# Performance work log

Measured on AMD Instinct MI355X. Metric: run time of the kernel, lower is better.

Reference implementation:

```python
import jax, jax.numpy as jnp
import numpy as np

C = 64          # residual channels
N_LAYERS = 30
MAX_STEPS = 200
SQRT2 = 2.0 ** 0.5


def _conv1d(x, W, b, dilation=1, pad=0):
    # x: [B, Cin, T], W: [Cout, Cin, K], b: [Cout]
    y = jax.lax.conv_general_dilated(
        x, W, window_strides=(1,), padding=[(pad, pad)],
        rhs_dilation=(dilation,), dimension_numbers=('NCH', 'OIH', 'NCH'))
    return y + b[None, :, None]


def _silu(x):
    return x * jax.nn.sigmoid(x)


def _emb_table():
    steps = jnp.arange(MAX_STEPS, dtype=jnp.float32)[:, None]      # [200,1]
    dims = jnp.arange(64, dtype=jnp.float32)[None, :]              # [1,64]
    t = steps * 10.0 ** (dims * 4.0 / 63.0)                        # [200,64]
    return jnp.concatenate([jnp.sin(t), jnp.cos(t)], axis=1)       # [200,128]


def setup_inputs() -> dict:
    key = jax.random.key(0)
    ks = jax.random.split(key, 20)
    B, T = 4, 16384
    f32 = jnp.float32
    inp = {
        'audio': jax.random.normal(ks[0], (B, 1, T), dtype=f32),
        'diffusion_step': jax.random.randint(ks[1], (B,), 0, MAX_STEPS),
        # input projection Conv1d(1, 64, 1)
        'in_W': jax.random.normal(ks[2], (C, 1, 1), f32) * 1.0,
        'in_b': jax.random.normal(ks[3], (C,), f32) * 0.01,
        # diffusion embedding MLP 128->512->512
        'p1_W': jax.random.normal(ks[4], (512, 128), f32) * (1.0 / np.sqrt(128)),
        'p1_b': jnp.zeros((512,), f32),
        'p2_W': jax.random.normal(ks[5], (512, 512), f32) * (1.0 / np.sqrt(512)),
        'p2_b': jnp.zeros((512,), f32),
        # per-layer params (stacked over 30 layers)
        'dw_W': jax.random.normal(ks[6], (N_LAYERS, 2 * C, C, 3), f32) * (1.0 / np.sqrt(3 * C)),
        'dw_b': jnp.zeros((N_LAYERS, 2 * C), f32),
        'dp_W': jax.random.normal(ks[7], (N_LAYERS, C, 512), f32) * (1.0 / np.sqrt(512)),
        'dp_b': jnp.zeros((N_LAYERS, C), f32),
        'op_W': jax.random.normal(ks[8], (N_LAYERS, 2 * C, C, 1), f32) * (1.0 / np.sqrt(C)),
        'op_b': jnp.zeros((N_LAYERS, 2 * C), f32),
        # skip projection Conv1d(64,64,1)
        'sk_W': jax.random.normal(ks[9], (C, C, 1), f32) * (1.0 / np.sqrt(C)),
        'sk_b': jnp.zeros((C,), f32),
        # output projection Conv1d(64,1,1), weight zero-init like original
        'out_W': jnp.zeros((1, C, 1), f32),
        'out_b': jax.random.normal(ks[10], (1,), f32) * 0.01,
    }
    return inp


def reference(audio, diffusion_step, in_W, in_b, p1_W, p1_b, p2_W, p2_b,
              dw_W, dw_b, dp_W, dp_b, op_W, op_b, sk_W, sk_b, out_W, out_b):
    x = jax.nn.relu(_conv1d(audio, in_W, in_b))                    # [B,64,T]
    # diffusion embedding
    t = _emb_table()[diffusion_step]                               # [B,128]
    t = _silu(t @ p1_W.T + p1_b)                                   # [B,512]
    t = _silu(t @ p2_W.T + p2_b)                                   # [B,512]
    skip = None
    for i in range(N_LAYERS):
        d = 2 ** (i % 10)
        cond = (t @ dp_W[i].T + dp_b[i])[:, :, None]               # [B,64,1]
        y = _conv1d(x + cond, dw_W[i], dw_b[i], dilation=d, pad=d) # [B,128,T]
        gate, filt = y[:, :C], y[:, C:]
        y = jax.nn.sigmoid(gate) * jnp.tanh(filt)                  # [B,64,T]
        y = _conv1d(y, op_W[i], op_b[i])                           # [B,128,T]
        residual, sk = y[:, :C], y[:, C:]
        x = (x + residual) / SQRT2
        skip = sk if skip is None else skip + sk
    x = skip / np.sqrt(float(N_LAYERS)).astype(np.float32)
    x = jax.nn.relu(_conv1d(x, sk_W, sk_b))
    return _conv1d(x, out_W, out_b)                                # [B,1,T]
```

## Files before the change

kernel.cpp:

```cpp
#include <hip/hip_runtime.h>
#include <math.h>

#define C 64
#define NL 30
#define T 16384
#define B 4

typedef __bf16 bf16_t;
typedef __bf16 bf16x8 __attribute__((ext_vector_type(8)));
typedef __bf16 bf16x4 __attribute__((ext_vector_type(4)));
typedef float f32x4 __attribute__((ext_vector_type(4)));

typedef const __attribute__((address_space(1))) unsigned int glb_u32;
typedef __attribute__((address_space(3))) unsigned int lds_u32;

constexpr float INV_SQRT2   = 0.70710678118654752440f;
constexpr float INV_SQRT_NL = 0.18257418583505537115f;

__device__ __forceinline__ float fsig(float x) {
    return __builtin_amdgcn_rcpf(1.f + __builtin_amdgcn_exp2f(-1.44269504089f * x));
}
__device__ __forceinline__ float ftanh(float x) {
    return fmaf(2.f, __builtin_amdgcn_rcpf(1.f + __builtin_amdgcn_exp2f(-2.88539008178f * x)), -1.f);
}
__device__ __forceinline__ int swz(int off) { return off ^ ((off >> 3) & 0x70); }

__global__ void pack_weights(const float* __restrict__ dw_W,
                             const float* __restrict__ op_W,
                             const float* __restrict__ sk_W,
                             bf16_t* __restrict__ convpk,
                             bf16_t* __restrict__ oppk,
                             bf16_t* __restrict__ skpk) {
    int idx = blockIdx.x * 256 + threadIdx.x;
    const int ndw = NL * 128 * 192;
    const int nop = NL * 128 * 64;
    if (idx < ndw) {
        int k = idx % 192; int r = idx / 192;
        int oc = r % 128;  int l = r / 128;
        int tap = k >> 6, ic = k & 63;
        convpk[idx] = (bf16_t)dw_W[((l * 128 + oc) * 64 + ic) * 3 + tap];
    } else if (idx < ndw + nop) {
        oppk[idx - ndw] = (bf16_t)op_W[idx - ndw];
    } else if (idx < ndw + nop + 4096) {
        int j = idx - ndw - nop;
        skpk[j] = (bf16_t)(sk_W[j] * INV_SQRT_NL);
    }
}

__global__ void cond_embp1(const int* __restrict__ step,
                           const float* __restrict__ p1_W, const float* __restrict__ p1_b,
                           float* __restrict__ h1out) {
    __shared__ float e[128];
    __shared__ float red[256];
    int b = blockIdx.x, blk = blockIdx.y, tid = threadIdx.x;
    int s = step[b];
    if (tid < 128) {
        int d = tid & 63;
        float tf = (float)s * powf(10.f, (float)d * 4.f / 63.f);
        double td = (double)tf;
        e[tid] = (tid < 64) ? (float)sin(td) : (float)cos(td);
    }
    __syncthreads();
    int ol = tid >> 2, q = tid & 3;
    int o = blk * 64 + ol;
    const float4* wr = (const float4*)(p1_W + o * 128 + q * 32);
    const float4* ev = (const float4*)(e + q * 32);
    float a = 0.f;
    #pragma unroll
    for (int j = 0; j < 8; ++j) {
        float4 wv = wr[j]; float4 xv = ev[j];
        a = fmaf(wv.x, xv.x, a); a = fmaf(wv.y, xv.y, a);
        a = fmaf(wv.z, xv.z, a); a = fmaf(wv.w, xv.w, a);
    }
    red[tid] = a;
    __syncthreads();
    if (q == 0) {
        float v = red[tid] + red[tid + 1] + red[tid + 2] + red[tid + 3] + p1_b[o];
        h1out[b * 512 + o] = v / (1.f + expf(-v));
    }
}

__global__ void cond_p2(const float* __restrict__ h1,
                        const float* __restrict__ p2_W, const float* __restrict__ p2_b,
                        float* __restrict__ h2out) {
    __shared__ float red[256];
    int b = blockIdx.x, blk = blockIdx.y, tid = threadIdx.x;
    int ol = tid >> 2, q = tid & 3;
    int o = blk * 64 + ol;
    const float4* wr = (const float4*)(p2_W + o * 512 + q * 128);
    const float4* hv = (const float4*)(h1 + b * 512 + q * 128);
    float a = 0.f;
    #pragma unroll 8
    for (int j = 0; j < 32; ++j) {
        float4 wv = wr[j]; float4 xv = hv[j];
        a = fmaf(wv.x, xv.x, a); a = fmaf(wv.y, xv.y, a);
        a = fmaf(wv.z, xv.z, a); a = fmaf(wv.w, xv.w, a);
    }
    red[tid] = a;
    __syncthreads();
    if (q == 0) {
        float v = red[tid] + red[tid + 1] + red[tid + 2] + red[tid + 3] + p2_b[o];
        h2out[b * 512 + o] = v / (1.f + expf(-v));
    }
}

__global__ void cond_stage2b(const float* __restrict__ h2,
                             const float* __restrict__ dp_W, const float* __restrict__ dp_b,
                             const bf16_t* __restrict__ convpk,
                             const float* __restrict__ dw_b,
                             float* __restrict__ bias2) {
    __shared__ float red[256];
    __shared__ float cond_s[64];
    int l = blockIdx.x, b = blockIdx.y;
    int tid = threadIdx.x;
    {
        int o = tid >> 2, q = tid & 3;
        const float4* wr = (const float4*)(dp_W + ((size_t)l * C + o) * 512 + q * 128);
        const float4* h = (const float4*)(h2 + b * 512 + q * 128);
        float a = 0.f;
        #pragma unroll 8
        for (int j = 0; j < 32; ++j) {
            float4 wv = wr[j]; float4 hv = h[j];
            a = fmaf(wv.x, hv.x, a); a = fmaf(wv.y, hv.y, a);
            a = fmaf(wv.z, hv.z, a); a = fmaf(wv.w, hv.w, a);
        }
        red[tid] = a;
        __syncthreads();
        if (q == 0)
            cond_s[o] = red[tid] + red[tid + 1] + red[tid + 2] + red[tid + 3] + dp_b[l * C + o];
    }
    __syncthreads();
    int oc = tid & 127, kh = tid >> 7;
    const bf16_t* wr = convpk + ((size_t)l * 128 + oc) * 192 + kh * 96;
    float a = kh ? 0.f : dw_b[l * 128 + oc];
    #pragma unroll
    for (int j = 0; j < 96; ++j)
        a = fmaf((float)wr[j], cond_s[(kh * 96 + j) & 63], a);
    __syncthreads();
    red[tid] = a;
    __syncthreads();
    if (tid < 128)
        bias2[(l * B + b) * 128 + tid] = red[tid] + red[tid + 128];
}

__global__ void in_conv(const float* __restrict__ audio,
                        const float* __restrict__ in_W, const float* __restrict__ in_b,
                        bf16_t* __restrict__ x) {
    int idx = blockIdx.x * 256 + threadIdx.x;
    int cb = idx & 7;
    int t = (idx >> 3) & (T - 1);
    int b = idx >> 17;
    float av = audio[b * T + t];
    bf16x8 o;
    #pragma unroll
    for (int j = 0; j < 8; ++j) {
        int c = cb * 8 + j;
        o[j] = (bf16_t)fmaxf(fmaf(in_W[c], av, in_b[c]), 0.f);
    }
    *(bf16x8*)(x + ((size_t)b * T + t) * 64 + cb * 8) = o;
}

__global__ __launch_bounds__(256) void layer_kernel(
    const bf16_t* __restrict__ x_in, bf16_t* __restrict__ x_out, bf16_t* __restrict__ skip,
    const bf16_t* __restrict__ convpk, const bf16_t* __restrict__ oppk,
    const float* __restrict__ bias2, const float* __restrict__ op_b,
    const bf16_t* __restrict__ zpage,
    int layer, int dil, int first)
{
    extern __shared__ char sm[];

    int tid = threadIdx.x;
    int w = __builtin_amdgcn_readfirstlane(tid >> 6);
    int l = tid & 63;
    int lr = l & 15;
    int g = l >> 4;
    int b = blockIdx.y;
    int tbase = blockIdx.x * 128;
    const bf16_t* xb = x_in + (size_t)b * T * 64;
    const bool dual = (dil <= 32);
    const int R = (dil <= 16) ? 3 : 4;

#define STAGE_SLAB(Sbase, t0s, RR)                                           \
    _Pragma("unroll")                                                        \
    for (int r = 0; r < (RR); ++r) {                                         \
        int row = r * 32 + (tid >> 3), c16 = tid & 7;                        \
        int ts = (t0s) - dil + row;                                          \
        int c16s = c16 ^ (row & 7);                                          \
        const bf16_t* src = ((unsigned)ts < (unsigned)T)                     \
            ? xb + (size_t)ts * 64 + c16s * 8 : zpage + c16s * 8;            \
        __builtin_amdgcn_global_load_lds((glb_u32*)src,                      \
            (lds_u32*)(sm + (Sbase) + r * 4096 + w * 1024), 16, 0, 0);       \
    }
#define STAGE_M3(t0s)                                                        \
    _Pragma("unroll")                                                        \
    for (int it = 0; it < 6; ++it) {                                         \
        int qq = it * 256 + tid;                                             \
        int slice = qq >> 9, row = (qq >> 3) & 63, c16 = qq & 7;             \
        int ts = (t0s) + row + (slice - 1) * dil;                            \
        int c16s = c16 ^ (row & 7);                                          \
        const bf16_t* src = ((unsigned)ts < (unsigned)T)                     \
            ? xb + (size_t)ts * 64 + c16s * 8 : zpage + c16s * 8;            \
        __builtin_amdgcn_global_load_lds((glb_u32*)src,                      \
            (lds_u32*)(sm + it * 4096 + w * 1024), 16, 0, 0);                \
    }

    if (dual) {
        if (dil <= 16) {
            STAGE_SLAB(0, tbase, 3)
            STAGE_SLAB(12288, tbase + 64, 3)
            asm volatile("s_waitcnt vmcnt(3)" ::: "memory");
        } else {
            STAGE_SLAB(0, tbase, 4)
            STAGE_SLAB(16384, tbase + 64, 4)
            asm volatile("s_waitcnt vmcnt(4)" ::: "memory");
        }
        __builtin_amdgcn_s_barrier();
        __builtin_amdgcn_sched_barrier(0);
    }

    bf16x8 cA[2][6];
    const bf16_t* cw = convpk + (size_t)layer * 128 * 192;
    #pragma unroll
    for (int mf = 0; mf < 2; ++mf)
        #pragma unroll
        for (int kf = 0; kf < 6; ++kf)
            cA[mf][kf] = *(const bf16x8*)(cw + (mf * 64 + w * 16 + lr) * 192 + kf * 32 + g * 8);
    bf16x8 oA[2][2];
    const bf16_t* ow = oppk + (size_t)layer * 128 * 64;
    #pragma unroll
    for (int mf = 0; mf < 2; ++mf)
        #pragma unroll
        for (int kf = 0; kf < 2; ++kf)
            oA[mf][kf] = *(const bf16x8*)(ow + (mf * 64 + w * 16 + lr) * 64 + kf * 32 + g * 8);
    f32x4 bC[2], bO[2];
    const float* b2 = bias2 + (layer * B + b) * 128;
    const float* ob = op_b + layer * 2 * C;
    #pragma unroll
    for (int mf = 0; mf < 2; ++mf)
        #pragma unroll
        for (int r = 0; r < 4; ++r) {
            bC[mf][r] = b2[mf * 64 + w * 16 + g * 4 + r];
            bO[mf][r] = ob[mf * 64 + w * 16 + g * 4 + r];
        }

    size_t bb = (size_t)b * T * 64;
    const int zb = dual ? 2 * R * 4096 : 24576;
    const int tapstride = dual ? dil * 128 : 8192;

    for (int st = 0; st < 2; ++st) {
        int Sb = dual ? st * R * 4096 : 0;
        int t0 = tbase + st * 64;

        if (!dual) {
            STAGE_M3(t0)
            __syncthreads();
        }

        f32x4 acc[2][4];
        #pragma unroll
        for (int mf = 0; mf < 2; ++mf)
            #pragma unroll
            for (int nf = 0; nf < 4; ++nf) acc[mf][nf] = bC[mf];
        #pragma unroll
        for (int kf = 0; kf < 6; ++kf) {
            int tap = kf >> 1;
            int kc = (kf & 1) * 32;
            bf16x8 Bf[4];
            #pragma unroll
            for (int nf = 0; nf < 4; ++nf) {
                int off = Sb + tap * tapstride + (nf * 16 + lr) * 128 + (kc + g * 8) * 2;
                Bf[nf] = *(const bf16x8*)(sm + swz(off));
            }
            #pragma unroll
            for (int mf = 0; mf < 2; ++mf)
                #pragma unroll
                for (int nf = 0; nf < 4; ++nf)
                    acc[mf][nf] = __builtin_amdgcn_mfma_f32_16x16x32_bf16(
                        cA[mf][kf], Bf[nf], acc[mf][nf], 0, 0, 0);
        }

        #pragma unroll
        for (int nf = 0; nf < 4; ++nf) {
            union { bf16_t hh[4]; uint2 u; } zp;
            #pragma unroll
            for (int r = 0; r < 4; ++r)
                zp.hh[r] = (bf16_t)(fsig(acc[0][nf][r]) * ftanh(acc[1][nf][r]));
            int off = zb + (nf * 16 + lr) * 128 + (w * 16 + g * 4) * 2;
            *(uint2*)(sm + swz(off)) = zp.u;
        }
        __syncthreads();

        f32x4 acc2[2][4];
        #pragma unroll
        for (int mf = 0; mf < 2; ++mf)
            #pragma unroll
            for (int nf = 0; nf < 4; ++nf) acc2[mf][nf] = bO[mf];
        #pragma unroll
        for (int kf = 0; kf < 2; ++kf) {
            bf16x8 Zf[4];
            #pragma unroll
            for (int nf = 0; nf < 4; ++nf) {
                int off = zb + (nf * 16 + lr) * 128 + (kf * 32 + g * 8) * 2;
                Zf[nf] = *(const bf16x8*)(sm + swz(off));
            }
            #pragma unroll
            for (int mf = 0; mf < 2; ++mf)
                #pragma unroll
                for (int nf = 0; nf < 4; ++nf)
                    acc2[mf][nf] = __builtin_amdgcn_mfma_f32_16x16x32_bf16(
                        oA[mf][kf], Zf[nf], acc2[mf][nf], 0, 0, 0);
        }

        #pragma unroll
        for (int nf = 0; nf < 4; ++nf) {
            int t = t0 + nf * 16 + lr;
            int c0 = w * 16 + g * 4;
            int xoff = Sb + tapstride + (nf * 16 + lr) * 128 + c0 * 2;
            bf16x4 xv = *(const bf16x4*)(sm + swz(xoff));
            bf16x4 ro, so;
            bf16_t* sp = skip + bb + (size_t)t * 64 + c0;
            if (first) {
                #pragma unroll
                for (int r = 0; r < 4; ++r) {
                    ro[r] = (bf16_t)(((float)xv[r] + acc2[0][nf][r]) * INV_SQRT2);
                    so[r] = (bf16_t)acc2[1][nf][r];
                }
            } else {
                bf16x4 sv = *(const bf16x4*)sp;
                #pragma unroll
                for (int r = 0; r < 4; ++r) {
                    ro[r] = (bf16_t)(((float)xv[r] + acc2[0][nf][r]) * INV_SQRT2);
                    so[r] = (bf16_t)((float)sv[r] + acc2[1][nf][r]);
                }
            }
            *(bf16x4*)(x_out + bb + (size_t)t * 64 + c0) = ro;
            *(bf16x4*)sp = so;
        }
        if (st == 0) __syncthreads();
    }
#undef STAGE_SLAB
#undef STAGE_M3
}

__global__ __launch_bounds__(256) void final_kernel(
    const bf16_t* __restrict__ skip, const bf16_t* __restrict__ skpk,
    const float* __restrict__ sk_b,
    const float* __restrict__ out_W, const float* __restrict__ out_b,
    float* __restrict__ out)
{
    __shared__ uint4 tile_u[512];
    __shared__ float part[16][66];
    unsigned char* sm = (unsigned char*)tile_u;
    int tid = threadIdx.x;
    int w = __builtin_amdgcn_readfirstlane(tid >> 6);
    int l = tid & 63, lr = l & 15, g = l >> 4;
    int b = blockIdx.y, t0 = blockIdx.x * 64;
    const bf16_t* sb = skip + (size_t)b * T * 64;

    #pragma unroll
    for (int it = 0; it < 2; ++it) {
        int q = it * 256 + tid;
        int row = q >> 3, c16 = q & 7;
        uint4 val = *(const uint4*)(sb + (size_t)(t0 + row) * 64 + c16 * 8);
        *(uint4*)(sm + swz(row * 128 + c16 * 16)) = val;
    }

    bf16x8 aS[2];
    #pragma unroll
    for (int kf = 0; kf < 2; ++kf)
        aS[kf] = *(const bf16x8*)(skpk + (w * 16 + lr) * 64 + kf * 32 + g * 8);
    f32x4 acc[4];
    #pragma unroll
    for (int nf = 0; nf < 4; ++nf)
        #pragma unroll
        for (int r = 0; r < 4; ++r) acc[nf][r] = sk_b[w * 16 + g * 4 + r];
    __syncthreads();

    #pragma unroll
    for (int kf = 0; kf < 2; ++kf) {
        bf16x8 Bf[4];
        #pragma unroll
        for (int nf = 0; nf < 4; ++nf) {
            int off = (nf * 16 + lr) * 128 + (kf * 32 + g * 8) * 2;
            Bf[nf] = *(const bf16x8*)(sm + swz(off));
        }
        #pragma unroll
        for (int nf = 0; nf < 4; ++nf)
            acc[nf] = __builtin_amdgcn_mfma_f32_16x16x32_bf16(aS[kf], Bf[nf], acc[nf], 0, 0, 0);
    }

    #pragma unroll
    for (int nf = 0; nf < 4; ++nf) {
        float o = 0.f;
        #pragma unroll
        for (int r = 0; r < 4; ++r)
            o = fmaf(out_W[w * 16 + g * 4 + r], fmaxf(acc[nf][r], 0.f), o);
        part[w * 4 + g][nf * 16 + lr] = o;
    }
    __syncthreads();
    if (tid < 64) {
        float o = out_b[0];
        #pragma unroll
        for (int j = 0; j < 16; ++j) o += part[j][tid];
        out[(size_t)b * T + t0 + tid] = o;
    }
}

extern "C" void kernel_launch(void* const* d_in, const int* in_sizes, int n_in,
                              void* d_out, int out_size, void* d_ws, size_t ws_size,
                              hipStream_t stream) {
    const float* audio = (const float*)d_in[0];
    const int*   dstep = (const int*)d_in[1];
    const float* in_W  = (const float*)d_in[2];
    const float* in_b  = (const float*)d_in[3];
    const float* p1_W  = (const float*)d_in[4];
    const float* p1_b  = (const float*)d_in[5];
    const float* p2_W  = (const float*)d_in[6];
    const float* p2_b  = (const float*)d_in[7];
    const float* dw_W  = (const float*)d_in[8];
    const float* dw_b  = (const float*)d_in[9];
    const float* dp_W  = (const float*)d_in[10];
    const float* dp_b  = (const float*)d_in[11];
    const float* op_W  = (const float*)d_in[12];
    const float* op_b  = (const float*)d_in[13];
    const float* sk_W  = (const float*)d_in[14];
    const float* sk_b  = (const float*)d_in[15];
    const float* out_W = (const float*)d_in[16];
    const float* out_b = (const float*)d_in[17];

    float* ws = (float*)d_ws;
    const size_t NXE = (size_t)B * T * 64;
    float* h1    = ws;
    float* h2    = h1 + B * 512;
    float* bias2 = h2 + B * 512;
    float* zpg   = bias2 + NL * B * 128;
    bf16_t* xA   = (bf16_t*)(zpg + 128);
    bf16_t* xB   = xA + NXE;
    bf16_t* skip = xB + NXE;
    bf16_t* convpk = skip + NXE;
    bf16_t* oppk   = convpk + (size_t)NL * 128 * 192;
    bf16_t* skpk   = oppk + (size_t)NL * 128 * 64;

    hipMemsetAsync(zpg, 0, 512, stream);
    hipLaunchKernelGGL(pack_weights, dim3(3856), dim3(256), 0, stream,
                       dw_W, op_W, sk_W, convpk, oppk, skpk);
    hipLaunchKernelGGL(cond_embp1, dim3(B, 8), dim3(256), 0, stream,
                       dstep, p1_W, p1_b, h1);
    hipLaunchKernelGGL(cond_p2, dim3(B, 8), dim3(256), 0, stream,
                       h1, p2_W, p2_b, h2);
    hipLaunchKernelGGL(cond_stage2b, dim3(NL, B), dim3(256), 0, stream,
                       h2, dp_W, dp_b, convpk, dw_b, bias2);
    hipLaunchKernelGGL(in_conv, dim3(B * T * 8 / 256), dim3(256), 0, stream,
                       audio, in_W, in_b, xA);
    for (int i = 0; i < NL; ++i) {
        bf16_t* xin  = (i & 1) ? xB : xA;
        bf16_t* xout = (i & 1) ? xA : xB;
        int dil = 1 << (i % 10);
        int shmem = (dil <= 16) ? 32768 : (dil <= 32 ? 40960 : 32768);
        hipLaunchKernelGGL(layer_kernel, dim3(T / 128, B), dim3(256), shmem, stream,
                           xin, xout, skip, convpk, oppk, bias2, op_b,
                           (const bf16_t*)zpg, i, dil, (i == 0) ? 1 : 0);
    }
    hipLaunchKernelGGL(final_kernel, dim3(T / 64, B), dim3(256), 0, stream,
                       skip, skpk, sk_b, out_W, out_b, (float*)d_out);
}
```

Measured before the change: 499.5 us.

## Fuse pairs of small-dilation WaveNet layers into one kernel with halo recompute

Layers with dilation up to 32 are now processed in pairs inside one templated kernel. The first layer's output, including halo rows, stays in LDS and the second layer consumes it directly, while skip contributions are accumulated in registers. This is meant to halve global round-trips of the activation and skip tensors and the number of launches for those layers, at the cost of redundant halo computation and more LDS. The remaining large-dilation layers keep a simplified three-slice staging path, and block indices are remapped to spread tiles across the grid.

```diff
diff --git a/kernel.cpp b/kernel.cpp
--- a/kernel.cpp
+++ b/kernel.cpp
@@ -167,7 +167,8 @@
     const bf16_t* __restrict__ zpage,
     int layer, int dil, int first)
 {
-    extern __shared__ char sm[];
+    __shared__ uint4 smem_u[2048];
+    char* sm = (char*)smem_u;
 
     int tid = threadIdx.x;
     int w = __builtin_amdgcn_readfirstlane(tid >> 6);
@@ -175,48 +176,10 @@
     int lr = l & 15;
     int g = l >> 4;
     int b = blockIdx.y;
-    int tbase = blockIdx.x * 128;
+    int bid = blockIdx.x;
+    int tile = ((bid & 7) << 4) + (bid >> 3);
+    int tbase = tile * 128;
     const bf16_t* xb = x_in + (size_t)b * T * 64;
-    const bool dual = (dil <= 32);
-    const int R = (dil <= 16) ? 3 : 4;
-
-#define STAGE_SLAB(Sbase, t0s, RR)                                           \
-    _Pragma("unroll")                                                        \
-    for (int r = 0; r < (RR); ++r) {                                         \
-        int row = r * 32 + (tid >> 3), c16 = tid & 7;                        \
-        int ts = (t0s) - dil + row;                                          \
-        int c16s = c16 ^ (row & 7);                                          \
-        const bf16_t* src = ((unsigned)ts < (unsigned)T)                     \
-            ? xb + (size_t)ts * 64 + c16s * 8 : zpage + c16s * 8;            \
-        __builtin_amdgcn_global_load_lds((glb_u32*)src,                      \
-            (lds_u32*)(sm + (Sbase) + r * 4096 + w * 1024), 16, 0, 0);       \
-    }
-#define STAGE_M3(t0s)                                                        \
-    _Pragma("unroll")                                                        \
-    for (int it = 0; it < 6; ++it) {                                         \
-        int qq = it * 256 + tid;                                             \
-        int slice = qq >> 9, row = (qq >> 3) & 63, c16 = qq & 7;             \
-        int ts = (t0s) + row + (slice - 1) * dil;                            \
-        int c16s = c16 ^ (row & 7);                                          \
-        const bf16_t* src = ((unsigned)ts < (unsigned)T)                     \
-            ? xb + (size_t)ts * 64 + c16s * 8 : zpage + c16s * 8;            \
-        __builtin_amdgcn_global_load_lds((glb_u32*)src,                      \
-            (lds_u32*)(sm + it * 4096 + w * 1024), 16, 0, 0);                \
-    }
-
-    if (dual) {
-        if (dil <= 16) {
-            STAGE_SLAB(0, tbase, 3)
-            STAGE_SLAB(12288, tbase + 64, 3)
-            asm volatile("s_waitcnt vmcnt(3)" ::: "memory");
-        } else {
-            STAGE_SLAB(0, tbase, 4)
-            STAGE_SLAB(16384, tbase + 64, 4)
-            asm volatile("s_waitcnt vmcnt(4)" ::: "memory");
-        }
-        __builtin_amdgcn_s_barrier();
-        __builtin_amdgcn_sched_barrier(0);
-    }
 
     bf16x8 cA[2][6];
     const bf16_t* cw = convpk + (size_t)layer * 128 * 192;
@@ -244,17 +207,23 @@
         }
 
     size_t bb = (size_t)b * T * 64;
-    const int zb = dual ? 2 * R * 4096 : 24576;
-    const int tapstride = dual ? dil * 128 : 8192;
 
     for (int st = 0; st < 2; ++st) {
-        int Sb = dual ? st * R * 4096 : 0;
         int t0 = tbase + st * 64;
 
-        if (!dual) {
-            STAGE_M3(t0)
-            __syncthreads();
-        }
+        #pragma unroll
+        for (int it = 0; it < 6; ++it) {
+            int qq = it * 256 + tid;
+            int slice = qq >> 9, row = (qq >> 3) & 63, c16 = qq & 7;
+            int ts = t0 + row + (slice - 1) * dil;
+            int c16s = c16 ^ (row & 7);
+            const bf16_t* src = ((unsigned)ts < (unsigned)T)
+                ? (xb + (size_t)ts * 64 + c16s * 8)
+                : (zpage + c16s * 8);
+            __builtin_amdgcn_global_load_lds((glb_u32*)src,
+                (lds_u32*)(sm + it * 4096 + w * 1024), 16, 0, 0);
+        }
+        __syncthreads();
 
         f32x4 acc[2][4];
         #pragma unroll
@@ -268,7 +237,7 @@
             bf16x8 Bf[4];
             #pragma unroll
             for (int nf = 0; nf < 4; ++nf) {
-                int off = Sb + tap * tapstride + (nf * 16 + lr) * 128 + (kc + g * 8) * 2;
+                int off = tap * 8192 + (nf * 16 + lr) * 128 + (kc + g * 8) * 2;
                 Bf[nf] = *(const bf16x8*)(sm + swz(off));
             }
             #pragma unroll
@@ -285,7 +254,7 @@
             #pragma unroll
             for (int r = 0; r < 4; ++r)
                 zp.hh[r] = (bf16_t)(fsig(acc[0][nf][r]) * ftanh(acc[1][nf][r]));
-            int off = zb + (nf * 16 + lr) * 128 + (w * 16 + g * 4) * 2;
+            int off = 24576 + (nf * 16 + lr) * 128 + (w * 16 + g * 4) * 2;
             *(uint2*)(sm + swz(off)) = zp.u;
         }
         __syncthreads();
@@ -300,7 +269,7 @@
             bf16x8 Zf[4];
             #pragma unroll
             for (int nf = 0; nf < 4; ++nf) {
-                int off = zb + (nf * 16 + lr) * 128 + (kf * 32 + g * 8) * 2;
+                int off = 24576 + (nf * 16 + lr) * 128 + (kf * 32 + g * 8) * 2;
                 Zf[nf] = *(const bf16x8*)(sm + swz(off));
             }
             #pragma unroll
@@ -315,7 +284,7 @@
         for (int nf = 0; nf < 4; ++nf) {
             int t = t0 + nf * 16 + lr;
             int c0 = w * 16 + g * 4;
-            int xoff = Sb + tapstride + (nf * 16 + lr) * 128 + c0 * 2;
+            int xoff = 8192 + (nf * 16 + lr) * 128 + c0 * 2;
             bf16x4 xv = *(const bf16x4*)(sm + swz(xoff));
             bf16x4 ro, so;
             bf16_t* sp = skip + bb + (size_t)t * 64 + c0;
@@ -338,8 +307,267 @@
         }
         if (st == 0) __syncthreads();
     }
-#undef STAGE_SLAB
-#undef STAGE_M3
+}
+
+template<int D1, int D2, int YOFF, int NYR, int XOFF, int NXR>
+__global__ __launch_bounds__(256) void fused_pair(
+    const bf16_t* __restrict__ x_in, bf16_t* __restrict__ x_out,
+    bf16_t* __restrict__ skip,
+    const bf16_t* __restrict__ convpk, const bf16_t* __restrict__ oppk,
+    const float* __restrict__ bias2, const float* __restrict__ op_b,
+    const bf16_t* __restrict__ zpage, int layerA, int first)
+{
+    extern __shared__ char sm[];
+    constexpr int NYF = NYR / 16;
+    constexpr int CF  = YOFF / 16;
+    constexpr int YS  = NXR * 128;
+    constexpr int ZS  = YS + NYR * 128;
+
+    int tid = threadIdx.x;
+    int w = __builtin_amdgcn_readfirstlane(tid >> 6);
+    int l = tid & 63, lr = l & 15, g = l >> 4;
+    int bid = blockIdx.x;
+    int tile = ((bid & 7) << 5) + (bid >> 3);
+    int b = blockIdx.y;
+    int t0 = tile * 64;
+    size_t bb = (size_t)b * T * 64;
+    const bf16_t* xb = x_in + bb;
+    int c0 = w * 16 + g * 4;
+
+    #pragma unroll
+    for (int r = 0; r < NXR / 32; ++r) {
+        int row = r * 32 + (tid >> 3), c16 = tid & 7;
+        int ts = t0 - XOFF + row;
+        int c16s = c16 ^ (row & 7);
+        const bf16_t* src = ((unsigned)ts < (unsigned)T)
+            ? (xb + (size_t)ts * 64 + c16s * 8)
+            : (zpage + c16s * 8);
+        __builtin_amdgcn_global_load_lds((glb_u32*)src,
+            (lds_u32*)(sm + r * 4096 + w * 1024), 16, 0, 0);
+    }
+
+    float skr[16];
+    #pragma unroll
+    for (int i = 0; i < 16; ++i) skr[i] = 0.f;
+
+    bf16x8 cA[2][6];
+    {
+        const bf16_t* cw = convpk + (size_t)layerA * 128 * 192;
+        #pragma unroll
+        for (int mf = 0; mf < 2; ++mf)
+            #pragma unroll
+            for (int kf = 0; kf < 6; ++kf)
+                cA[mf][kf] = *(const bf16x8*)(cw + (mf * 64 + w * 16 + lr) * 192 + kf * 32 + g * 8);
+    }
+    bf16x8 oA[2][2];
+    {
+        const bf16_t* ow = oppk + (size_t)layerA * 128 * 64;
+        #pragma unroll
+        for (int mf = 0; mf < 2; ++mf)
+            #pragma unroll
+            for (int kf = 0; kf < 2; ++kf)
+                oA[mf][kf] = *(const bf16x8*)(ow + (mf * 64 + w * 16 + lr) * 64 + kf * 32 + g * 8);
+    }
+    f32x4 bC[2], bO[2];
+    {
+        const float* b2 = bias2 + (layerA * B + b) * 128;
+        const float* ob = op_b + layerA * 2 * C;
+        #pragma unroll
+        for (int mf = 0; mf < 2; ++mf)
+            #pragma unroll
+            for (int r = 0; r < 4; ++r) {
+                bC[mf][r] = b2[mf * 64 + c0 + r];
+                bO[mf][r] = ob[mf * 64 + c0 + r];
+            }
+    }
+    __syncthreads();
+
+    f32x4 acc[2][NYF];
+    #pragma unroll
+    for (int mf = 0; mf < 2; ++mf)
+        #pragma unroll
+        for (int nf = 0; nf < NYF; ++nf) acc[mf][nf] = bC[mf];
+    #pragma unroll
+    for (int kf = 0; kf < 6; ++kf) {
+        int tap = kf >> 1;
+        int kc = (kf & 1) * 32;
+        bf16x8 Bf[NYF];
+        #pragma unroll
+        for (int nf = 0; nf < NYF; ++nf) {
+            int ix = (nf * 16 + lr) + (XOFF - YOFF) + (tap - 1) * D1;
+            Bf[nf] = *(const bf16x8*)(sm + swz(ix * 128 + (kc + g * 8) * 2));
+        }
+        #pragma unroll
+        for (int mf = 0; mf < 2; ++mf)
+            #pragma unroll
+            for (int nf = 0; nf < NYF; ++nf)
+                acc[mf][nf] = __builtin_amdgcn_mfma_f32_16x16x32_bf16(
+                    cA[mf][kf], Bf[nf], acc[mf][nf], 0, 0, 0);
+    }
+
+    #pragma unroll
+    for (int nf = 0; nf < NYF; ++nf) {
+        union { bf16_t hh[4]; uint2 u; } zp;
+        #pragma unroll
+        for (int r = 0; r < 4; ++r)
+            zp.hh[r] = (bf16_t)(fsig(acc[0][nf][r]) * ftanh(acc[1][nf][r]));
+        int off = ZS + (nf * 16 + lr) * 128 + c0 * 2;
+        *(uint2*)(sm + swz(off)) = zp.u;
+    }
+    __syncthreads();
+
+    {
+        f32x4 acc2[2][NYF];
+        #pragma unroll
+        for (int mf = 0; mf < 2; ++mf)
+            #pragma unroll
+            for (int nf = 0; nf < NYF; ++nf) acc2[mf][nf] = bO[mf];
+        #pragma unroll
+        for (int kf = 0; kf < 2; ++kf) {
+            bf16x8 Zf[NYF];
+            #pragma unroll
+            for (int nf = 0; nf < NYF; ++nf) {
+                int off = ZS + (nf * 16 + lr) * 128 + (kf * 32 + g * 8) * 2;
+                Zf[nf] = *(const bf16x8*)(sm + swz(off));
+            }
+            #pragma unroll
+            for (int mf = 0; mf < 2; ++mf)
+                #pragma unroll
+                for (int nf = 0; nf < NYF; ++nf)
+                    acc2[mf][nf] = __builtin_amdgcn_mfma_f32_16x16x32_bf16(
+                        oA[mf][kf], Zf[nf], acc2[mf][nf], 0, 0, 0);
+        }
+        #pragma unroll
+        for (int nf = 0; nf < NYF; ++nf) {
+            int iy = nf * 16 + lr;
+            int ta = t0 - YOFF + iy;
+            bool inr = ((unsigned)ta < (unsigned)T);
+            int ixc = iy + (XOFF - YOFF);
+            bf16x4 xv = *(const bf16x4*)(sm + swz(ixc * 128 + c0 * 2));
+            bf16x4 yo;
+            #pragma unroll
+            for (int r = 0; r < 4; ++r) {
+                float yv = ((float)xv[r] + acc2[0][nf][r]) * INV_SQRT2;
+                yo[r] = inr ? (bf16_t)yv : (bf16_t)0.f;
+                if (nf >= CF && nf < CF + 4)
+                    skr[(nf - CF) * 4 + r] += acc2[1][nf][r];
+            }
+            *(bf16x4*)(sm + swz(YS + iy * 128 + c0 * 2)) = yo;
+        }
+    }
+
+    int layerB = layerA + 1;
+    bf16x8 cB[2][6];
+    {
+        const bf16_t* cw = convpk + (size_t)layerB * 128 * 192;
+        #pragma unroll
+        for (int mf = 0; mf < 2; ++mf)
+            #pragma unroll
+            for (int kf = 0; kf < 6; ++kf)
+                cB[mf][kf] = *(const bf16x8*)(cw + (mf * 64 + w * 16 + lr) * 192 + kf * 32 + g * 8);
+    }
+    bf16x8 oB[2][2];
+    {
+        const bf16_t* ow = oppk + (size_t)layerB * 128 * 64;
+        #pragma unroll
+        for (int mf = 0; mf < 2; ++mf)
+            #pragma unroll
+            for (int kf = 0; kf < 2; ++kf)
+                oB[mf][kf] = *(const bf16x8*)(ow + (mf * 64 + w * 16 + lr) * 64 + kf * 32 + g * 8);
+    }
+    f32x4 bCB[2], bOB[2];
+    {
+        const float* b2 = bias2 + (layerB * B + b) * 128;
+        const float* ob = op_b + layerB * 2 * C;
+        #pragma unroll
+        for (int mf = 0; mf < 2; ++mf)
+            #pragma unroll
+            for (int r = 0; r < 4; ++r) {
+                bCB[mf][r] = b2[mf * 64 + c0 + r];
+                bOB[mf][r] = ob[mf * 64 + c0 + r];
+            }
+    }
+    __syncthreads();
+
+    f32x4 accB[2][4];
+    #pragma unroll
+    for (int mf = 0; mf < 2; ++mf)
+        #pragma unroll
+        for (int nf = 0; nf < 4; ++nf) accB[mf][nf] = bCB[mf];
+    #pragma unroll
+    for (int kf = 0; kf < 6; ++kf) {
+        int tap = kf >> 1;
+        int kc = (kf & 1) * 32;
+        bf16x8 Bf[4];
+        #pragma unroll
+        for (int nf = 0; nf < 4; ++nf) {
+            int jy = (nf * 16 + lr) + YOFF + (tap - 1) * D2;
+            Bf[nf] = *(const bf16x8*)(sm + swz(YS + jy * 128 + (kc + g * 8) * 2));
+        }
+        #pragma unroll
+        for (int mf = 0; mf < 2; ++mf)
+            #pragma unroll
+            for (int nf = 0; nf < 4; ++nf)
+                accB[mf][nf] = __builtin_amdgcn_mfma_f32_16x16x32_bf16(
+                    cB[mf][kf], Bf[nf], accB[mf][nf], 0, 0, 0);
+    }
+
+    #pragma unroll
+    for (int nf = 0; nf < 4; ++nf) {
+        union { bf16_t hh[4]; uint2 u; } zp;
+        #pragma unroll
+        for (int r = 0; r < 4; ++r)
+            zp.hh[r] = (bf16_t)(fsig(accB[0][nf][r]) * ftanh(accB[1][nf][r]));
+        int off = ZS + (nf * 16 + lr) * 128 + c0 * 2;
+        *(uint2*)(sm + swz(off)) = zp.u;
+    }
+    __syncthreads();
+
+    f32x4 acc2B[2][4];
+    #pragma unroll
+    for (int mf = 0; mf < 2; ++mf)
+        #pragma unroll
+        for (int nf = 0; nf < 4; ++nf) acc2B[mf][nf] = bOB[mf];
+    #pragma unroll
+    for (int kf = 0; kf < 2; ++kf) {
+        bf16x8 Zf[4];
+        #pragma unroll
+        for (int nf = 0; nf < 4; ++nf) {
+            int off = ZS + (nf * 16 + lr) * 128 + (kf * 32 + g * 8) * 2;
+            Zf[nf] = *(const bf16x8*)(sm + swz(off));
+        }
+        #pragma unroll
+        for (int mf = 0; mf < 2; ++mf)
+            #pragma unroll
+            for (int nf = 0; nf < 4; ++nf)
+                acc2B[mf][nf] = __builtin_amdgcn_mfma_f32_16x16x32_bf16(
+                    oB[mf][kf], Zf[nf], acc2B[mf][nf], 0, 0, 0);
+    }
+    #pragma unroll
+    for (int nf = 0; nf < 4; ++nf) {
+        int it = nf * 16 + lr;
+        int t = t0 + it;
+        int jyc = it + YOFF;
+        bf16x4 yv = *(const bf16x4*)(sm + swz(YS + jyc * 128 + c0 * 2));
+        bf16x4 ro, so;
+        bf16_t* sp = skip + bb + (size_t)t * 64 + c0;
+        if (first) {
+            #pragma unroll
+            for (int r = 0; r < 4; ++r) {
+                ro[r] = (bf16_t)(((float)yv[r] + acc2B[0][nf][r]) * INV_SQRT2);
+                so[r] = (bf16_t)(skr[nf * 4 + r] + acc2B[1][nf][r]);
+            }
+        } else {
+            bf16x4 sv = *(const bf16x4*)sp;
+            #pragma unroll
+            for (int r = 0; r < 4; ++r) {
+                ro[r] = (bf16_t)(((float)yv[r] + acc2B[0][nf][r]) * INV_SQRT2);
+                so[r] = (bf16_t)((float)sv[r] + skr[nf * 4 + r] + acc2B[1][nf][r]);
+            }
+        }
+        *(bf16x4*)(x_out + bb + (size_t)t * 64 + c0) = ro;
+        *(bf16x4*)sp = so;
+    }
 }
 
 __global__ __launch_bounds__(256) void final_kernel(
@@ -354,7 +582,9 @@
     int tid = threadIdx.x;
     int w = __builtin_amdgcn_readfirstlane(tid >> 6);
     int l = tid & 63, lr = l & 15, g = l >> 4;
-    int b = blockIdx.y, t0 = blockIdx.x * 64;
+    int bid = blockIdx.x;
+    int tile = ((bid & 7) << 5) + (bid >> 3);
+    int b = blockIdx.y, t0 = tile * 64;
     const bf16_t* sb = skip + (size_t)b * T * 64;
 
     #pragma unroll
@@ -452,14 +682,34 @@
                        h2, dp_W, dp_b, convpk, dw_b, bias2);
     hipLaunchKernelGGL(in_conv, dim3(B * T * 8 / 256), dim3(256), 0, stream,
                        audio, in_W, in_b, xA);
-    for (int i = 0; i < NL; ++i) {
-        bf16_t* xin  = (i & 1) ? xB : xA;
-        bf16_t* xout = (i & 1) ? xA : xB;
-        int dil = 1 << (i % 10);
-        int shmem = (dil <= 16) ? 32768 : (dil <= 32 ? 40960 : 32768);
-        hipLaunchKernelGGL(layer_kernel, dim3(T / 128, B), dim3(256), shmem, stream,
-                           xin, xout, skip, convpk, oppk, bias2, op_b,
-                           (const bf16_t*)zpg, i, dil, (i == 0) ? 1 : 0);
+
+    bf16_t* bufs[2] = { xA, xB };
+    int cur = 0;
+    const bf16_t* zpgc = (const bf16_t*)zpg;
+    for (int dec = 0; dec < 3; ++dec) {
+        int base = dec * 10;
+        hipLaunchKernelGGL((fused_pair<1, 2, 16, 96, 32, 128>),
+                           dim3(T / 64, B), dim3(256), 40960, stream,
+                           bufs[cur], bufs[cur ^ 1], skip, convpk, oppk,
+                           bias2, op_b, zpgc, base + 0, (dec == 0) ? 1 : 0);
+        cur ^= 1;
+        hipLaunchKernelGGL((fused_pair<4, 8, 16, 96, 32, 128>),
+                           dim3(T / 64, B), dim3(256), 40960, stream,
+                           bufs[cur], bufs[cur ^ 1], skip, convpk, oppk,
+                           bias2, op_b, zpgc, base + 2, 0);
+        cur ^= 1;
+        hipLaunchKernelGGL((fused_pair<16, 32, 32, 128, 48, 160>),
+                           dim3(T / 64, B), dim3(256), 53248, stream,
+                           bufs[cur], bufs[cur ^ 1], skip, convpk, oppk,
+                           bias2, op_b, zpgc, base + 4, 0);
+        cur ^= 1;
+        for (int j = 6; j < 10; ++j) {
+            int dil = 1 << j;
+            hipLaunchKernelGGL(layer_kernel, dim3(T / 128, B), dim3(256), 0, stream,
+                               bufs[cur], bufs[cur ^ 1], skip, convpk, oppk,
+                               bias2, op_b, zpgc, base + j, dil, 0);
+            cur ^= 1;
+        }
     }
     hipLaunchKernelGGL(final_kernel, dim3(T / 64, B), dim3(256), 0, stream,
                        skip, skpk, sk_b, out_W, out_b, (float*)d_out);
```

Result: faster. 467.7 us (-6.4%).
